# Optimization experiments

Measured on AMD Instinct MI355X. Metric: run time of the kernel, lower is better.

Reference implementation:

```python
import jax, jax.numpy as jnp
import numpy as np

N_HEADS = 32
N_KV = 8
HEAD_DIM = 64
GROUP = N_HEADS // N_KV  # 4


def setup_inputs() -> dict:
    key = jax.random.key(0)
    ks = jax.random.split(key, 6)
    b, s, d_in, d_out = 1, 4096, 2048, 2048
    d_kv = N_KV * HEAD_DIM
    sc = 0.02
    return {
        'x': jax.random.normal(ks[0], (b, s, d_in), jnp.float32),
        'Wq': jax.random.normal(ks[1], (d_in, d_out), jnp.float32) * sc,
        'Wk': jax.random.normal(ks[2], (d_in, d_kv), jnp.float32) * sc,
        'Wv': jax.random.normal(ks[3], (d_in, d_kv), jnp.float32) * sc,
        'Wo': jax.random.normal(ks[4], (d_out, d_out), jnp.float32) * sc,
        'bo': jnp.zeros((d_out,), jnp.float32),
    }


def reference(x, Wq, Wk, Wv, Wo, bo):
    b, s, _ = x.shape
    # projections (no qkv bias)
    q = (x @ Wq).reshape(b, s, N_HEADS, HEAD_DIM).transpose(0, 2, 1, 3)  # [b,h,s,hd]
    k = (x @ Wk).reshape(b, s, N_KV, HEAD_DIM).transpose(0, 2, 1, 3)    # [b,g,s,hd]
    v = (x @ Wv).reshape(b, s, N_KV, HEAD_DIM).transpose(0, 2, 1, 3)
    # GQA: repeat kv heads (matches repeat_interleave on dim=1)
    k = jnp.repeat(k, GROUP, axis=1)  # [b,h,s,hd]
    v = jnp.repeat(v, GROUP, axis=1)
    scores = jnp.einsum('bhqd,bhkd->bhqk', q, k)
    causal = jnp.triu(jnp.ones((s, s), dtype=bool), k=1)
    scores = jnp.where(causal, -jnp.inf, scores)
    attn = jax.nn.softmax(scores / (HEAD_DIM ** 0.5), axis=-1)
    ctx = jnp.einsum('bhqk,bhkd->bhqd', attn, v)
    ctx = ctx.transpose(0, 2, 1, 3).reshape(b, s, N_HEADS * HEAD_DIM)
    return ctx @ Wo + bo
```

## Files before the change

### kernel.cpp

```cpp
#include <hip/hip_runtime.h>
#include <hip/hip_bf16.h>
#include <cstdint>


typedef unsigned int u32;
typedef unsigned short u16;
typedef __attribute__((ext_vector_type(8))) short bf16x8;
typedef __attribute__((ext_vector_type(4))) float f32x4;
typedef __attribute__((ext_vector_type(2))) u32 u32x2;

typedef __attribute__((address_space(3))) void lds_void_t;
typedef __attribute__((address_space(1))) void gbl_void_t;

__device__ __forceinline__ void gload_lds16(const u16* g, u16* l) {
    __builtin_amdgcn_global_load_lds((const gbl_void_t*)g, (lds_void_t*)l, 16, 0, 0);
}

__device__ __forceinline__ u16 f2bf(float f) {
    union { float f; u32 i; } c; c.f = f;
    return (u16)((c.i + 0x7fffu + ((c.i >> 16) & 1u)) >> 16);
}
__device__ __forceinline__ float bfround(float f) {
    union { float f; u32 i; } c; c.f = f;
    c.i = (c.i + 0x7fffu + ((c.i >> 16) & 1u)) & 0xffff0000u;
    return c.f;
}
__device__ __forceinline__ u32 packbf2(float a, float b) {
    union { __hip_bfloat162 h; u32 w; } c;
    c.h = __float22bfloat162_rn(make_float2(a, b));
    return c.w;
}

__global__ __launch_bounds__(256) void cast_f2b_kernel(
    const float* __restrict__ s, u16* __restrict__ d)
{
    int i = (blockIdx.x * 256 + threadIdx.x) * 8;
    float4 a = *reinterpret_cast<const float4*>(s + i);
    float4 b = *reinterpret_cast<const float4*>(s + i + 4);
    u32 w[4];
    w[0] = packbf2(a.x, a.y); w[1] = packbf2(a.z, a.w);
    w[2] = packbf2(b.x, b.y); w[3] = packbf2(b.z, b.w);
    *reinterpret_cast<uint4*>(d + i) = *reinterpret_cast<const uint4*>(w);
}

__global__ __launch_bounds__(256) void cast_transpose_kernel(
    const float* __restrict__ W, u16* __restrict__ Wt, int K, int N)
{
    __shared__ float tile[64][65];
    const int k0 = blockIdx.y * 64, n0 = blockIdx.x * 64;
    const int t = threadIdx.x;
#pragma unroll
    for (int i = 0; i < 16; ++i) {
        int idx = t + i * 256;
        int r = idx >> 6, c = idx & 63;
        tile[r][c] = W[(size_t)(k0 + r) * N + n0 + c];
    }
    __syncthreads();
#pragma unroll
    for (int i = 0; i < 16; ++i) {
        int idx = t + i * 256;
        int r = idx >> 6, c = idx & 63;
        Wt[(size_t)(n0 + r) * K + k0 + c] = f2bf(tile[c][r]);
    }
}

__global__ __launch_bounds__(256) void gemm_qkv_kernel(
    const u16* __restrict__ A, const u16* __restrict__ Bt,
    u16* __restrict__ Qw, u16* __restrict__ Kw, u16* __restrict__ Vtw,
    int M, int K, float qscale)
{
    __shared__ __align__(16) u16 As[2][128][32];
    __shared__ __align__(16) u16 Bs[2][128][32];

    const int tid  = threadIdx.x;
    const int wave = tid >> 6;
    const int lane = tid & 63;
    const int col  = lane & 15;
    const int quad = lane >> 4;
    const int bflat = (int)blockIdx.y * 24 + (int)blockIdx.x;
    const int nb_   = (bflat & 7) * 96 + (bflat >> 3);
    const int bm = (nb_ / 24) * 128, bn = (nb_ % 24) * 128;
    const int mhalf = (wave & 1) * 64, nhalf = (wave >> 1) * 64;

    const int srow = wave * 32 + (lane >> 2);
    const int skch = lane & 3;
    const u16* ga = A  + (size_t)(bm + srow) * K + skch * 8;
    const u16* gb = Bt + (size_t)(bn + srow) * K + skch * 8;
    const int w32 = wave * 32;

    f32x4 acc[4][4];
#pragma unroll
    for (int i = 0; i < 4; ++i)
#pragma unroll
        for (int j = 0; j < 4; ++j) acc[i][j] = (f32x4){0.f, 0.f, 0.f, 0.f};

    gload_lds16(ga, &As[0][w32][0]);
    gload_lds16(ga + 16 * K, &As[0][w32 + 16][0]);
    gload_lds16(gb, &Bs[0][w32][0]);
    gload_lds16(gb + 16 * K, &Bs[0][w32 + 16][0]);
    ga += 32; gb += 32;

    for (int k0 = 0; k0 < K; k0 += 32) {
        const int cur = (k0 >> 5) & 1;
        __syncthreads();

        if (k0 + 32 < K) {
            const int nb = cur ^ 1;
            gload_lds16(ga, &As[nb][w32][0]);
            gload_lds16(ga + 16 * K, &As[nb][w32 + 16][0]);
            gload_lds16(gb, &Bs[nb][w32][0]);
            gload_lds16(gb + 16 * K, &Bs[nb][w32 + 16][0]);
            ga += 32; gb += 32;
        }

        bf16x8 af[4], bf[4];
#pragma unroll
        for (int t = 0; t < 4; ++t)
            af[t] = *reinterpret_cast<const bf16x8*>(&As[cur][mhalf + t * 16 + col][quad * 8]);
#pragma unroll
        for (int t = 0; t < 4; ++t)
            bf[t] = *reinterpret_cast<const bf16x8*>(&Bs[cur][nhalf + t * 16 + col][quad * 8]);
#pragma unroll
        for (int tm = 0; tm < 4; ++tm)
#pragma unroll
            for (int tn = 0; tn < 4; ++tn)
                acc[tm][tn] = __builtin_amdgcn_mfma_f32_16x16x32_bf16(
                    af[tm], bf[tn], acc[tm][tn], 0, 0, 0);
    }

    if (bn < 2048) {
#pragma unroll
        for (int tm = 0; tm < 4; ++tm) {
            int row0 = bm + mhalf + tm * 16 + quad * 4;
#pragma unroll
            for (int r = 0; r < 4; ++r) {
                u16* cp = Qw + (size_t)(row0 + r) * 2048 + bn + nhalf + col;
#pragma unroll
                for (int tn = 0; tn < 4; ++tn)
                    cp[tn * 16] = f2bf(acc[tm][tn][r] * qscale);
            }
        }
    } else if (bn < 2560) {
        const int cb = bn - 2048;
#pragma unroll
        for (int tm = 0; tm < 4; ++tm) {
            int row0 = bm + mhalf + tm * 16 + quad * 4;
#pragma unroll
            for (int r = 0; r < 4; ++r) {
                u16* cp = Kw + (size_t)(row0 + r) * 512 + cb + nhalf + col;
#pragma unroll
                for (int tn = 0; tn < 4; ++tn)
                    cp[tn * 16] = f2bf(acc[tm][tn][r]);
            }
        }
    } else {
        const int cb = bn - 2560;
#pragma unroll
        for (int tn = 0; tn < 4; ++tn) {
            int nrow = cb + nhalf + tn * 16 + col;
#pragma unroll
            for (int tm = 0; tm < 4; ++tm) {
                int m0 = bm + mhalf + tm * 16 + quad * 4;
                ushort4 v;
                v.x = f2bf(acc[tm][tn][0]); v.y = f2bf(acc[tm][tn][1]);
                v.z = f2bf(acc[tm][tn][2]); v.w = f2bf(acc[tm][tn][3]);
                *reinterpret_cast<ushort4*>(&Vtw[(size_t)nrow * M + m0]) = v;
            }
        }
    }
}

__global__ __launch_bounds__(256) void gemm_out_kernel(
    const u16* __restrict__ A, const u16* __restrict__ Bt,
    const float* __restrict__ bias, float* __restrict__ Co,
    int M, int N, int K)
{
    __shared__ __align__(16) u16 As[2][128][32];
    __shared__ __align__(16) u16 Bs[2][128][32];

    const int tid  = threadIdx.x;
    const int wave = tid >> 6;
    const int lane = tid & 63;
    const int col  = lane & 15;
    const int quad = lane >> 4;
    const int bflat = (int)blockIdx.y * 16 + (int)blockIdx.x;
    const int nb_   = (bflat & 7) * 64 + (bflat >> 3);
    const int bm = (nb_ / 16) * 128, bn = (nb_ % 16) * 128;
    const int mhalf = (wave & 1) * 64, nhalf = (wave >> 1) * 64;

    const int srow = wave * 32 + (lane >> 2);
    const int skch = lane & 3;
    const u16* ga = A  + (size_t)(bm + srow) * K + skch * 8;
    const u16* gb = Bt + (size_t)(bn + srow) * K + skch * 8;
    const int w32 = wave * 32;

    f32x4 acc[4][4];
#pragma unroll
    for (int i = 0; i < 4; ++i)
#pragma unroll
        for (int j = 0; j < 4; ++j) acc[i][j] = (f32x4){0.f, 0.f, 0.f, 0.f};

    gload_lds16(ga, &As[0][w32][0]);
    gload_lds16(ga + 16 * K, &As[0][w32 + 16][0]);
    gload_lds16(gb, &Bs[0][w32][0]);
    gload_lds16(gb + 16 * K, &Bs[0][w32 + 16][0]);
    ga += 32; gb += 32;

    for (int k0 = 0; k0 < K; k0 += 32) {
        const int cur = (k0 >> 5) & 1;
        __syncthreads();

        if (k0 + 32 < K) {
            const int nb = cur ^ 1;
            gload_lds16(ga, &As[nb][w32][0]);
            gload_lds16(ga + 16 * K, &As[nb][w32 + 16][0]);
            gload_lds16(gb, &Bs[nb][w32][0]);
            gload_lds16(gb + 16 * K, &Bs[nb][w32 + 16][0]);
            ga += 32; gb += 32;
        }

        bf16x8 af[4], bf[4];
#pragma unroll
        for (int t = 0; t < 4; ++t)
            af[t] = *reinterpret_cast<const bf16x8*>(&As[cur][mhalf + t * 16 + col][quad * 8]);
#pragma unroll
        for (int t = 0; t < 4; ++t)
            bf[t] = *reinterpret_cast<const bf16x8*>(&Bs[cur][nhalf + t * 16 + col][quad * 8]);
#pragma unroll
        for (int tm = 0; tm < 4; ++tm)
#pragma unroll
            for (int tn = 0; tn < 4; ++tn)
                acc[tm][tn] = __builtin_amdgcn_mfma_f32_16x16x32_bf16(
                    af[tm], bf[tn], acc[tm][tn], 0, 0, 0);
    }

    float bj[4];
#pragma unroll
    for (int tn = 0; tn < 4; ++tn) bj[tn] = bias[bn + nhalf + tn * 16 + col];
#pragma unroll
    for (int tm = 0; tm < 4; ++tm) {
        int row0 = bm + mhalf + tm * 16 + quad * 4;
#pragma unroll
        for (int r = 0; r < 4; ++r) {
            float* cp = Co + (size_t)(row0 + r) * N + bn + nhalf + col;
#pragma unroll
            for (int tn = 0; tn < 4; ++tn)
                cp[tn * 16] = bfround(acc[tm][tn][r] + bj[tn]);
        }
    }
}

__global__ __launch_bounds__(256, 2) void attn_mfma_kernel(
    const u16* __restrict__ Q,
    const u16* __restrict__ Kd,
    const u16* __restrict__ Vt,
    u16* __restrict__ CTX,
    int S)
{
    __shared__ __align__(16) u16 Ks[2][128][64];
    __shared__ __align__(16) u16 Vs[2][64][128];
    __shared__ __align__(16) u32 Pu[4][1024];

    const int bflat = (int)blockIdx.y * 16 + (int)blockIdx.x;
    const int nbw   = (bflat & 7) * 64 + (bflat >> 3);
    const int h     = nbw >> 4;
    const int pairi = nbw & 15;
    const int g    = h >> 2;
    const int tid  = threadIdx.x;
    const int wave = tid >> 6;
    const int lane = tid & 63;
    const int col  = lane & 15;
    const int quad = lane >> 4;

    const int srow8 = lane >> 3;
    const int schk  = (lane & 7) ^ srow8;
    const u16* gK = Kd + (size_t)(wave * 32 + srow8) * 512 + g * 64 + schk * 8;

    const int vrow  = lane >> 4;
    const int vhalf = (lane >> 3) & 1;
    const int vchk0 = (lane & 7) ^ vrow;
    const u16* gVbase = Vt + (size_t)(g * 64 + wave * 16 + vrow) * 4096 + vhalf * 64;
    const u16* gV0 = gVbase + vchk0 * 8;
    const u16* gV1 = gVbase + (vchk0 ^ 4) * 8;

    const int wbase = ((quad >> 1) * 16 + col) * 4 + (quad & 1) * 2;

#pragma unroll 1
    for (int pass = 0; pass < 2; ++pass) {
        const int qt = pass ? pairi : (31 - pairi);
        const int qb = qt * 128;

        bf16x8 qf[2][2];
#pragma unroll
        for (int mt = 0; mt < 2; ++mt) {
            const u16* qp = Q + (size_t)(qb + wave * 32 + mt * 16 + col) * 2048
                            + h * 64 + quad * 8;
            qf[mt][0] = *reinterpret_cast<const bf16x8*>(qp);
            qf[mt][1] = *reinterpret_cast<const bf16x8*>(qp + 32);
        }

        f32x4 o_acc[2][4];
        float l_acc[2];
#pragma unroll
        for (int mt = 0; mt < 2; ++mt) {
            l_acc[mt] = 0.f;
#pragma unroll
            for (int t = 0; t < 4; ++t)
                o_acc[mt][t] = (f32x4){0.f, 0.f, 0.f, 0.f};
        }

        const int ktmax = qt;

        __syncthreads();
#pragma unroll
        for (int j = 0; j < 4; ++j) {
            gload_lds16(gK + (size_t)(j * 8) * 512, &Ks[0][wave * 32 + j * 8][0]);
            const u16* gv = (j & 1) ? gV1 : gV0;
            gload_lds16(gv + (size_t)(j * 4) * 4096, &Vs[0][wave * 16 + j * 4][0]);
        }

        for (int kt = 0; kt <= ktmax; ++kt) {
            const int cur = kt & 1;
            __syncthreads();

            if (kt < ktmax) {
                const int nb = cur ^ 1;
                const size_t ko = (size_t)(kt + 1) * 128;
#pragma unroll
                for (int j = 0; j < 4; ++j) {
                    gload_lds16(gK + (ko + j * 8) * 512, &Ks[nb][wave * 32 + j * 8][0]);
                    const u16* gv = (j & 1) ? gV1 : gV0;
                    gload_lds16(gv + ko + (size_t)(j * 4) * 4096, &Vs[nb][wave * 16 + j * 4][0]);
                }
            }

            const int base0 = qb + wave * 32;

#pragma unroll
            for (int h64 = 0; h64 < 2; ++h64) {
                const int kbase = kt * 128 + h64 * 64;
                if (kbase > base0 + 31) continue;
                const bool act0 = (kbase <= base0 + 15);
                const int rbase = h64 * 64;

                f32x4 sc0[4], sc1[4];
                __builtin_amdgcn_s_setprio(1);
#pragma unroll
                for (int t = 0; t < 4; ++t) {
                    const int krow = t * 16 + col;
                    bf16x8 k0 = *reinterpret_cast<const bf16x8*>(
                        &Ks[cur][rbase + krow][((quad    ) ^ (krow & 7)) * 8]);
                    bf16x8 k1 = *reinterpret_cast<const bf16x8*>(
                        &Ks[cur][rbase + krow][((quad + 4) ^ (krow & 7)) * 8]);
                    f32x4 c4 = {-16.f, -16.f, -16.f, -16.f};
                    c4 = __builtin_amdgcn_mfma_f32_16x16x32_bf16(k0, qf[1][0], c4, 0, 0, 0);
                    c4 = __builtin_amdgcn_mfma_f32_16x16x32_bf16(k1, qf[1][1], c4, 0, 0, 0);
                    sc1[t] = c4;
                    if (act0) {
                        f32x4 d4 = {-16.f, -16.f, -16.f, -16.f};
                        d4 = __builtin_amdgcn_mfma_f32_16x16x32_bf16(k0, qf[0][0], d4, 0, 0, 0);
                        d4 = __builtin_amdgcn_mfma_f32_16x16x32_bf16(k1, qf[0][1], d4, 0, 0, 0);
                        sc0[t] = d4;
                    }
                }
                __builtin_amdgcn_s_setprio(0);

                if (kbase + 63 > base0) {
#pragma unroll
                    for (int t = 0; t < 4; ++t) {
                        const int keyq = kbase + t * 16 + quad * 4;
#pragma unroll
                        for (int r = 0; r < 4; ++r) {
                            if (keyq + r > base0 + 16 + col) sc1[t][r] = -1e30f;
                            if (act0 && (keyq + r > base0 + col)) sc0[t][r] = -1e30f;
                        }
                    }
                }

                {
                    float ls0 = 0.f, ls1 = 0.f;
#pragma unroll
                    for (int t = 0; t < 4; ++t) {
                        float p0 = __builtin_amdgcn_exp2f(sc1[t][0]);
                        float p1 = __builtin_amdgcn_exp2f(sc1[t][1]);
                        float p2 = __builtin_amdgcn_exp2f(sc1[t][2]);
                        float p3 = __builtin_amdgcn_exp2f(sc1[t][3]);
                        ls1 += (p0 + p1) + (p2 + p3);
                        u32x2 w;
                        w.x = packbf2(p0, p1);
                        w.y = packbf2(p2, p3);
                        *reinterpret_cast<u32x2*>(&Pu[wave][512 + wbase + t * 128]) = w;
                        if (act0) {
                            float q0 = __builtin_amdgcn_exp2f(sc0[t][0]);
                            float q1 = __builtin_amdgcn_exp2f(sc0[t][1]);
                            float q2 = __builtin_amdgcn_exp2f(sc0[t][2]);
                            float q3 = __builtin_amdgcn_exp2f(sc0[t][3]);
                            ls0 += (q0 + q1) + (q2 + q3);
                            u32x2 v;
                            v.x = packbf2(q0, q1);
                            v.y = packbf2(q2, q3);
                            *reinterpret_cast<u32x2*>(&Pu[wave][wbase + t * 128]) = v;
                        }
                    }
                    l_acc[1] += ls1;
                    if (act0) l_acc[0] += ls0;
                }

                __builtin_amdgcn_s_waitcnt(0xC07F);
                __builtin_amdgcn_wave_barrier();

                bf16x8 pa1_0 = *reinterpret_cast<const bf16x8*>(&Pu[wave][512 + lane * 4]);
                bf16x8 pa1_1 = *reinterpret_cast<const bf16x8*>(&Pu[wave][768 + lane * 4]);
                bf16x8 pa0_0, pa0_1;
                if (act0) {
                    pa0_0 = *reinterpret_cast<const bf16x8*>(&Pu[wave][lane * 4]);
                    pa0_1 = *reinterpret_cast<const bf16x8*>(&Pu[wave][256 + lane * 4]);
                }

                __builtin_amdgcn_s_setprio(1);
#pragma unroll
                for (int t = 0; t < 4; ++t) {
                    const int d = t * 16 + col;
                    bf16x8 vb0 = *reinterpret_cast<const bf16x8*>(
                        &Vs[cur][d][rbase + ((quad    ) ^ (d & 7)) * 8]);
                    bf16x8 vb1 = *reinterpret_cast<const bf16x8*>(
                        &Vs[cur][d][rbase + ((quad + 4) ^ (d & 7)) * 8]);
                    o_acc[1][t] = __builtin_amdgcn_mfma_f32_16x16x32_bf16(pa1_0, vb0, o_acc[1][t], 0, 0, 0);
                    o_acc[1][t] = __builtin_amdgcn_mfma_f32_16x16x32_bf16(pa1_1, vb1, o_acc[1][t], 0, 0, 0);
                    if (act0) {
                        o_acc[0][t] = __builtin_amdgcn_mfma_f32_16x16x32_bf16(pa0_0, vb0, o_acc[0][t], 0, 0, 0);
                        o_acc[0][t] = __builtin_amdgcn_mfma_f32_16x16x32_bf16(pa0_1, vb1, o_acc[0][t], 0, 0, 0);
                    }
                }
                __builtin_amdgcn_s_setprio(0);
            }
        }

#pragma unroll
        for (int mt = 0; mt < 2; ++mt) {
            float v = l_acc[mt];
            v += __shfl_xor(v, 16, 64);
            v += __shfl_xor(v, 32, 64);
            const int src0 = (lane & 48) + ((lane >> 4) & 3) * 4;
#pragma unroll
            for (int r = 0; r < 4; ++r) {
                const float lv = __shfl(v, src0 + r, 64);
                const float inv = 1.f / lv;
                const int row = qb + wave * 32 + mt * 16 + quad * 4 + r;
                u16* cp = CTX + (size_t)row * 2048 + h * 64;
#pragma unroll
                for (int t = 0; t < 4; ++t)
                    cp[t * 16 + col] = f2bf(o_acc[mt][t][r] * inv);
            }
        }
    }
}

extern "C" void kernel_launch(void* const* d_in, const int* in_sizes, int n_in,
                              void* d_out, int out_size, void* d_ws, size_t ws_size,
                              hipStream_t stream)
{
    const float* x  = (const float*)d_in[0];
    const float* Wq = (const float*)d_in[1];
    const float* Wk = (const float*)d_in[2];
    const float* Wv = (const float*)d_in[3];
    const float* Wo = (const float*)d_in[4];
    const float* bo = (const float*)d_in[5];
    float* out = (float*)d_out;

    const int S = 4096, Din = 2048, Dq = 2048, Dkv = 512;
    const float QSCALE = 0.125f * 1.44269504f;

    u16* xb  = (u16*)d_ws;
    u16* Qw  = xb + (size_t)S * Din;
    u16* Kw  = Qw + (size_t)S * Dq;
    u16* Vtw = Kw + (size_t)S * Dkv;
    u16* Cw   = xb;
    u16* Wobt = Qw;

    u16* Wqkvt = (u16*)d_out;

    dim3 blk(256);
    cast_f2b_kernel<<<dim3((S * Din) / (256 * 8)), blk, 0, stream>>>(x, xb);
    cast_transpose_kernel<<<dim3(Dq  / 64, Din / 64), blk, 0, stream>>>(Wq, Wqkvt, Din, Dq);
    cast_transpose_kernel<<<dim3(Dkv / 64, Din / 64), blk, 0, stream>>>(Wk, Wqkvt + (size_t)2048 * Din, Din, Dkv);
    cast_transpose_kernel<<<dim3(Dkv / 64, Din / 64), blk, 0, stream>>>(Wv, Wqkvt + (size_t)2560 * Din, Din, Dkv);

    gemm_qkv_kernel<<<dim3(3072 / 128, S / 128), blk, 0, stream>>>(
        xb, Wqkvt, Qw, Kw, Vtw, S, Din, QSCALE);

    attn_mfma_kernel<<<dim3(16, 32), blk, 0, stream>>>(Qw, Kw, Vtw, Cw, S);

    cast_transpose_kernel<<<dim3(Dq / 64, Dq / 64), blk, 0, stream>>>(Wo, Wobt, Dq, Dq);
    gemm_out_kernel<<<dim3(Dq / 128, S / 128), blk, 0, stream>>>(Cw, Wobt, bo, out, S, Dq, Dq);
}
```

Measured before the change: 331.5 us.

## Triple-buffer LDS in QKV and output GEMMs with explicit vmcnt waits

```diff
diff --git a/kernel.cpp b/kernel.cpp
--- a/kernel.cpp
+++ b/kernel.cpp
@@ -69,8 +69,8 @@
     u16* __restrict__ Qw, u16* __restrict__ Kw, u16* __restrict__ Vtw,
     int M, int K, float qscale)
 {
-    __shared__ __align__(16) u16 As[2][128][32];
-    __shared__ __align__(16) u16 Bs[2][128][32];
+    __shared__ __align__(16) u16 As[3][128][32];
+    __shared__ __align__(16) u16 Bs[3][128][32];
 
     const int tid  = threadIdx.x;
     const int wave = tid >> 6;
@@ -94,22 +94,31 @@
 #pragma unroll
         for (int j = 0; j < 4; ++j) acc[i][j] = (f32x4){0.f, 0.f, 0.f, 0.f};
 
-    gload_lds16(ga, &As[0][w32][0]);
-    gload_lds16(ga + 16 * K, &As[0][w32 + 16][0]);
-    gload_lds16(gb, &Bs[0][w32][0]);
-    gload_lds16(gb + 16 * K, &Bs[0][w32 + 16][0]);
-    ga += 32; gb += 32;
-
+#pragma unroll
+    for (int p = 0; p < 2; ++p) {
+        gload_lds16(ga, &As[p][w32][0]);
+        gload_lds16(ga + 16 * K, &As[p][w32 + 16][0]);
+        gload_lds16(gb, &Bs[p][w32][0]);
+        gload_lds16(gb + 16 * K, &Bs[p][w32 + 16][0]);
+        ga += 32; gb += 32;
+    }
+
+    int cur = 0;
     for (int k0 = 0; k0 < K; k0 += 32) {
-        const int cur = (k0 >> 5) & 1;
-        __syncthreads();
-
         if (k0 + 32 < K) {
-            const int nb = cur ^ 1;
-            gload_lds16(ga, &As[nb][w32][0]);
-            gload_lds16(ga + 16 * K, &As[nb][w32 + 16][0]);
-            gload_lds16(gb, &Bs[nb][w32][0]);
-            gload_lds16(gb + 16 * K, &Bs[nb][w32 + 16][0]);
+            asm volatile("s_waitcnt vmcnt(4)" ::: "memory");
+        } else {
+            asm volatile("s_waitcnt vmcnt(0)" ::: "memory");
+        }
+        __builtin_amdgcn_s_barrier();
+        __builtin_amdgcn_sched_barrier(0);
+
+        if (k0 + 64 < K) {
+            const int sb = cur ? cur - 1 : 2;
+            gload_lds16(ga, &As[sb][w32][0]);
+            gload_lds16(ga + 16 * K, &As[sb][w32 + 16][0]);
+            gload_lds16(gb, &Bs[sb][w32][0]);
+            gload_lds16(gb + 16 * K, &Bs[sb][w32 + 16][0]);
             ga += 32; gb += 32;
         }
 
@@ -126,6 +135,8 @@
             for (int tn = 0; tn < 4; ++tn)
                 acc[tm][tn] = __builtin_amdgcn_mfma_f32_16x16x32_bf16(
                     af[tm], bf[tn], acc[tm][tn], 0, 0, 0);
+
+        cur = (cur == 2) ? 0 : cur + 1;
     }
 
     if (bn < 2048) {
@@ -175,8 +186,8 @@
     const float* __restrict__ bias, float* __restrict__ Co,
     int M, int N, int K)
 {
-    __shared__ __align__(16) u16 As[2][128][32];
-    __shared__ __align__(16) u16 Bs[2][128][32];
+    __shared__ __align__(16) u16 As[3][128][32];
+    __shared__ __align__(16) u16 Bs[3][128][32];
 
     const int tid  = threadIdx.x;
     const int wave = tid >> 6;
@@ -200,22 +211,31 @@
 #pragma unroll
         for (int j = 0; j < 4; ++j) acc[i][j] = (f32x4){0.f, 0.f, 0.f, 0.f};
 
-    gload_lds16(ga, &As[0][w32][0]);
-    gload_lds16(ga + 16 * K, &As[0][w32 + 16][0]);
-    gload_lds16(gb, &Bs[0][w32][0]);
-    gload_lds16(gb + 16 * K, &Bs[0][w32 + 16][0]);
-    ga += 32; gb += 32;
-
+#pragma unroll
+    for (int p = 0; p < 2; ++p) {
+        gload_lds16(ga, &As[p][w32][0]);
+        gload_lds16(ga + 16 * K, &As[p][w32 + 16][0]);
+        gload_lds16(gb, &Bs[p][w32][0]);
+        gload_lds16(gb + 16 * K, &Bs[p][w32 + 16][0]);
+        ga += 32; gb += 32;
+    }
+
+    int cur = 0;
     for (int k0 = 0; k0 < K; k0 += 32) {
-        const int cur = (k0 >> 5) & 1;
-        __syncthreads();
-
         if (k0 + 32 < K) {
-            const int nb = cur ^ 1;
-            gload_lds16(ga, &As[nb][w32][0]);
-            gload_lds16(ga + 16 * K, &As[nb][w32 + 16][0]);
-            gload_lds16(gb, &Bs[nb][w32][0]);
-            gload_lds16(gb + 16 * K, &Bs[nb][w32 + 16][0]);
+            asm volatile("s_waitcnt vmcnt(4)" ::: "memory");
+        } else {
+            asm volatile("s_waitcnt vmcnt(0)" ::: "memory");
+        }
+        __builtin_amdgcn_s_barrier();
+        __builtin_amdgcn_sched_barrier(0);
+
+        if (k0 + 64 < K) {
+            const int sb = cur ? cur - 1 : 2;
+            gload_lds16(ga, &As[sb][w32][0]);
+            gload_lds16(ga + 16 * K, &As[sb][w32 + 16][0]);
+            gload_lds16(gb, &Bs[sb][w32][0]);
+            gload_lds16(gb + 16 * K, &Bs[sb][w32 + 16][0]);
             ga += 32; gb += 32;
         }
 
@@ -232,6 +252,8 @@
             for (int tn = 0; tn < 4; ++tn)
                 acc[tm][tn] = __builtin_amdgcn_mfma_f32_16x16x32_bf16(
                     af[tm], bf[tn], acc[tm][tn], 0, 0, 0);
+
+        cur = (cur == 2) ? 0 : cur + 1;
     }
 
     float bj[4];
```

After: 332.4 us. Within noise of the previous version (+0.3%).
